# Performance work log

Measured on AMD Instinct MI355X. Metric: run time of the kernel, lower is better.

## Reference

```python
import jax, jax.numpy as jnp
import numpy as np

D_MODEL = 1024
N_HEADS = 16
D_HEAD = D_MODEL // N_HEADS
ROPE_BASE = 10000.0


def setup_inputs() -> dict:
    key = jax.random.key(0)
    k1, k2, k3, k4, k5 = jax.random.split(key, 5)
    std = 0.02 / np.sqrt(2 * 12)  # scaled_xavier with n_layers=12
    x = jax.random.normal(k1, (2, 2048, D_MODEL), dtype=jnp.float32)
    qkv_w = jax.random.normal(k2, (3 * D_MODEL, D_MODEL), dtype=jnp.float32) * std
    qkv_b = jnp.zeros((3 * D_MODEL,), dtype=jnp.float32)
    proj_w = jax.random.normal(k3, (D_MODEL, D_MODEL), dtype=jnp.float32) * std
    proj_b = jnp.zeros((D_MODEL,), dtype=jnp.float32)
    return {"x": x, "qkv_w": qkv_w, "qkv_b": qkv_b, "proj_w": proj_w, "proj_b": proj_b}


def _rope_cos_sin(seq_len, dtype):
    inv_freq = 1.0 / (ROPE_BASE ** (jnp.arange(0, D_HEAD, 2, dtype=jnp.float32) / D_HEAD))
    t = jnp.arange(seq_len, dtype=jnp.float32)
    freqs = jnp.einsum("t,d->td", t, inv_freq)          # [S, Dh/2]
    freqs = jnp.concatenate([freqs, freqs], axis=-1)      # [S, Dh]
    return jnp.cos(freqs).astype(dtype), jnp.sin(freqs).astype(dtype)


def _rotate_half(x):
    x1, x2 = jnp.split(x, 2, axis=-1)
    return jnp.concatenate([-x2, x1], axis=-1)


def reference(x, qkv_w, qkv_b, proj_w, proj_b):
    B, S, D = x.shape
    H, Dh = N_HEADS, D_HEAD
    scale = 1.0 / np.sqrt(Dh)

    qkv = x @ qkv_w.T + qkv_b                              # [B, S, 3D]
    qkv = qkv.reshape(B, S, 3, H, Dh)
    q = jnp.transpose(qkv[:, :, 0], (0, 2, 1, 3))          # [B, H, S, Dh]
    k = jnp.transpose(qkv[:, :, 1], (0, 2, 1, 3))
    v = jnp.transpose(qkv[:, :, 2], (0, 2, 1, 3))

    cos, sin = _rope_cos_sin(S, x.dtype)                   # [S, Dh]
    q = q * cos + _rotate_half(q) * sin
    k = k * cos + _rotate_half(k) * sin

    scores = jnp.einsum("bhsd,bhtd->bhst", q, k) * scale   # [B, H, S, S]
    causal = jnp.triu(jnp.ones((S, S), dtype=bool), k=1)
    neg = jnp.finfo(scores.dtype).min
    scores = jnp.where(causal[None, None], neg, scores)

    probs = jax.nn.softmax(scores, axis=-1)
    ctx = jnp.einsum("bhst,bhtd->bhsd", probs, v)          # [B, H, S, Dh]
    out = jnp.transpose(ctx, (0, 2, 1, 3)).reshape(B, S, D)
    out = out @ proj_w.T + proj_b
    return out
```

## Files before the change

### kernel.cpp

```cpp
#include <hip/hip_runtime.h>
#include <hip/hip_bf16.h>

#define BATCH 2
#define SEQ   2048
#define DMODEL 1024
#define NHEADS 16
#define DHEAD  64
#define MTOT   (BATCH * SEQ)
#define QKSTR  2048

typedef __attribute__((ext_vector_type(8))) short bf16x8;
typedef __attribute__((ext_vector_type(4))) float f32x4;

__device__ __forceinline__ void glds16(const void* g, void* l)
{
    __builtin_amdgcn_global_load_lds(
        (const __attribute__((address_space(1))) unsigned int*)g,
        (__attribute__((address_space(3))) unsigned int*)l, 16, 0, 0);
}

__global__ void cast_all_kernel(
    const float* __restrict__ a, __hip_bfloat16* __restrict__ oa, int na4,
    const float* __restrict__ b, __hip_bfloat16* __restrict__ ob, int nb4,
    const float* __restrict__ c, __hip_bfloat16* __restrict__ oc, int nc4)
{
    int i = blockIdx.x * blockDim.x + threadIdx.x;
    const float* src; __hip_bfloat16* dst; int j = i;
    if (j < na4) { src = a; dst = oa; }
    else {
        j -= na4;
        if (j < nb4) { src = b; dst = ob; }
        else {
            j -= nb4;
            if (j >= nc4) return;
            src = c; dst = oc;
        }
    }
    float4 v = ((const float4*)src)[j];
    __hip_bfloat16 tmp[4];
    tmp[0] = __float2bfloat16(v.x);
    tmp[1] = __float2bfloat16(v.y);
    tmp[2] = __float2bfloat16(v.z);
    tmp[3] = __float2bfloat16(v.w);
    *(uint2*)(dst + 4 * (size_t)j) = *(const uint2*)tmp;
}

#define GTM 128
#define GBK 64

__device__ __forceinline__ void store_out(float* p, float v) { *p = v; }
__device__ __forceinline__ void store_out(__hip_bfloat16* p, float v) { *p = __float2bfloat16(v); }

template <typename OutT, int MODE, int TN>
__global__ __launch_bounds__(256) void gemm_bias_kernel(
    const __hip_bfloat16* __restrict__ A, const __hip_bfloat16* __restrict__ W,
    const float* __restrict__ bias, OutT* __restrict__ out,
    __hip_bfloat16* __restrict__ vtg,
    int M, int N, int K)
{
    const int NI = TN / 32;
    const int bm = blockIdx.x * GTM;
    const int bn = blockIdx.y * TN;
    const int tid = threadIdx.x;
    const int wave = tid >> 6;
    const int lane = tid & 63;
    const int quad = lane >> 4;
    const int l16 = lane & 15;
    const int wm = (wave & 1) * 64;
    const int wn = (wave >> 1) * (TN / 2);

    __shared__ __hip_bfloat16 As[GTM * GBK];
    __shared__ __hip_bfloat16 Bs[TN * GBK];

    f32x4 acc[4][NI] = {};

    const int srow = lane >> 3;
    const int gc8 = (((lane & 7) ^ srow)) * 8;

    for (int kt = 0; kt < K; kt += GBK) {
#pragma unroll
        for (int t = 0; t < 4; t++) {
            int i = wave * 4 + t;
            glds16(A + (size_t)(bm + i * 8 + srow) * K + kt + gc8, As + i * 512);
        }
#pragma unroll
        for (int t = 0; t < TN / 32; t++) {
            int i = wave * (TN / 32) + t;
            glds16(W + (size_t)(bn + i * 8 + srow) * K + kt + gc8, Bs + i * 512);
        }
        __syncthreads();

#pragma unroll
        for (int kk = 0; kk < 2; kk++) {
            bf16x8 af[4], bfr[NI];
#pragma unroll
            for (int i = 0; i < 4; i++) {
                int ra = wm + i * 16 + l16;
                af[i] = *(const bf16x8*)(As + ra * 64 + (((kk << 2) + quad) ^ (ra & 7)) * 8);
            }
#pragma unroll
            for (int i = 0; i < NI; i++) {
                int rb = wn + i * 16 + l16;
                bfr[i] = *(const bf16x8*)(Bs + rb * 64 + (((kk << 2) + quad) ^ (rb & 7)) * 8);
            }
#pragma unroll
            for (int mi = 0; mi < 4; mi++)
#pragma unroll
                for (int ni = 0; ni < NI; ni++)
                    acc[mi][ni] = __builtin_amdgcn_mfma_f32_16x16x32_bf16(
                        af[mi], bfr[ni], acc[mi][ni], 0, 0, 0);
        }
        __syncthreads();
    }

    if (MODE == 1 && (bn + wn) < 2 * DMODEL) {
#pragma unroll
        for (int ni = 0; ni < 2; ni++) {
            int col = bn + wn + ni * 16 + l16;
            int i32 = col & 31;
            float invf = exp2f(-13.287712379549449f * (float)i32 * (1.0f / 32.0f));
            float b1 = bias[col], b2 = bias[col + 32];
#pragma unroll
            for (int mi = 0; mi < 4; mi++) {
#pragma unroll
                for (int r = 0; r < 4; r++) {
                    int row = bm + wm + mi * 16 + quad * 4 + r;
                    int s = row & (SEQ - 1);
                    float ang = (float)s * invf;
                    float sn, cs;
                    __sincosf(ang, &sn, &cs);
                    float x1 = acc[mi][ni][r] + b1;
                    float x2 = acc[mi][ni + 2][r] + b2;
                    store_out(&out[(size_t)row * QKSTR + col], x1 * cs - x2 * sn);
                    store_out(&out[(size_t)row * QKSTR + col + 32], x2 * cs + x1 * sn);
                }
            }
        }
    } else if (MODE == 1) {
#pragma unroll
        for (int ni = 0; ni < NI; ni++) {
            int colg = bn + wn + ni * 16 + l16;
            int vcol = colg - 2 * DMODEL;
            int hh = vcol >> 6, dh = vcol & 63;
            float bv = bias[colg];
#pragma unroll
            for (int mi = 0; mi < 4; mi++) {
                int row0 = bm + wm + mi * 16 + quad * 4;
                int bb = row0 >> 11;
                int ss = row0 & (SEQ - 1);
                __hip_bfloat16 tmp[4];
#pragma unroll
                for (int r = 0; r < 4; r++)
                    tmp[r] = __float2bfloat16(acc[mi][ni][r] + bv);
                *(uint2*)(vtg + (((size_t)bb * NHEADS + hh) * DHEAD + dh) * SEQ + ss) =
                    *(uint2*)tmp;
            }
        }
    } else {
#pragma unroll
        for (int mi = 0; mi < 4; mi++)
#pragma unroll
            for (int ni = 0; ni < NI; ni++) {
                int col = bn + wn + ni * 16 + l16;
                float bv = bias[col];
#pragma unroll
                for (int r = 0; r < 4; r++) {
                    int row = bm + wm + mi * 16 + quad * 4 + r;
                    store_out(&out[(size_t)row * N + col], acc[mi][ni][r] + bv);
                }
            }
    }
}

__global__ __launch_bounds__(512, 2) void flash_attn_mfma_kernel(
    const __hip_bfloat16* __restrict__ qkb,
    const __hip_bfloat16* __restrict__ vtg,
    __hip_bfloat16* __restrict__ ctx)
{
    const int bh = blockIdx.x;
    const int b = bh >> 4, h = bh & 15;
    const int y = blockIdx.y;
    const int qa = y, qb = 15 - y;
    const int tid = threadIdx.x;
    const int w = tid >> 6;
    const int lane = tid & 63;
    const int quad = lane >> 4;
    const int l16 = lane & 15;
    const int band = w & 3;
    const int qt = (w >> 2) ? qb : qa;
    const int jmax_w = 2 * qt + (band >> 1);
    const int jmax_b = 2 * qb + 1;

    __shared__ __hip_bfloat16 Ks[2][64 * 64];
    __shared__ __hip_bfloat16 Vt[2][64 * 64];
    __shared__ __hip_bfloat16 Ps[256 * 64];

    const __hip_bfloat16* qbase = qkb + (size_t)b * SEQ * QKSTR + h * DHEAD;
    const __hip_bfloat16* kbase = qbase + DMODEL;
    const __hip_bfloat16* vbase = vtg + (size_t)bh * DHEAD * SEQ;

    bf16x8 qf[2][2];
#pragma unroll
    for (int mi = 0; mi < 2; mi++) {
        const __hip_bfloat16* qr =
            qbase + (size_t)(qt * 128 + band * 32 + mi * 16 + l16) * QKSTR;
        qf[mi][0] = *(const bf16x8*)(qr + quad * 8);
        qf[mi][1] = *(const bf16x8*)(qr + 32 + quad * 8);
    }

    const int srow = lane >> 3;
    const int gc8 = ((lane & 7) ^ srow) * 8;
    const __hip_bfloat16* kg = kbase + (size_t)(w * 8 + srow) * QKSTR + gc8;
    const __hip_bfloat16* vg = vbase + (size_t)(w * 8 + srow) * SEQ + gc8;

    const int xr = l16 & 7;
    const int fo0 = l16 * 64 + ((quad ^ xr) << 3);
    const int fo1 = l16 * 64 + (((4 + quad) ^ xr) << 3);
    const int pbase = w * 32;

    const short onev = (l16 == 0) ? (short)0x3F80 : (short)0;
    const bf16x8 ones = {onev, onev, onev, onev, onev, onev, onev, onev};

    glds16(kg, &Ks[0][w * 512]);
    glds16(vg, &Vt[0][w * 512]);

    f32x4 oacc[2][5] = {};

    for (int jt = 0; jt <= jmax_b; jt++) {
        __syncthreads();
        const int cur = jt & 1;
        if (jt < jmax_b) {
            glds16(kg + (size_t)(jt + 1) * 64 * QKSTR, &Ks[cur ^ 1][w * 512]);
            glds16(vg + (jt + 1) * 64, &Vt[cur ^ 1][w * 512]);
        }
        if (jt <= jmax_w) {
            const __hip_bfloat16* ks = Ks[cur];
            const __hip_bfloat16* vs = Vt[cur];

            f32x4 s4[2][4] = {};
#pragma unroll
            for (int kk = 0; kk < 2; kk++) {
                const int fo = kk ? fo1 : fo0;
                bf16x8 kf[4];
#pragma unroll
                for (int nt = 0; nt < 4; nt++)
                    kf[nt] = *(const bf16x8*)(ks + nt * 1024 + fo);
#pragma unroll
                for (int mi = 0; mi < 2; mi++)
#pragma unroll
                    for (int nt = 0; nt < 4; nt++)
                        s4[mi][nt] = __builtin_amdgcn_mfma_f32_16x16x32_bf16(
                            qf[mi][kk], kf[nt], s4[mi][nt], 0, 0, 0);
            }

            const int k0 = jt * 64;
#pragma unroll
            for (int mi = 0; mi < 2; mi++) {
                const int qmin = qt * 128 + band * 32 + mi * 16;
                const bool needmask = (k0 + 63) > qmin;
#pragma unroll
                for (int nt = 0; nt < 4; nt++)
#pragma unroll
                    for (int r = 0; r < 4; r++) {
                        float p = __expf(s4[mi][nt][r] * 0.125f);
                        if (needmask)
                            p = (k0 + nt * 16 + l16 <= qmin + quad * 4 + r) ? p : 0.f;
                        int rr = quad * 4 + r;
                        Ps[(pbase + mi * 16 + rr) * 64 +
                           (((nt * 2 + (l16 >> 3)) ^ (rr & 7)) << 3) + xr] =
                            __float2bfloat16(p);
                    }
            }

#pragma unroll
            for (int kk = 0; kk < 2; kk++) {
                const int fo = kk ? fo1 : fo0;
                bf16x8 pf[2];
#pragma unroll
                for (int mi = 0; mi < 2; mi++)
                    pf[mi] = *(const bf16x8*)(Ps + (pbase + mi * 16 + l16) * 64 +
                                              ((((kk << 2) + quad) ^ xr) << 3));
#pragma unroll
                for (int dt = 0; dt < 4; dt++) {
                    bf16x8 vf = *(const bf16x8*)(vs + dt * 1024 + fo);
#pragma unroll
                    for (int mi = 0; mi < 2; mi++)
                        oacc[mi][dt] = __builtin_amdgcn_mfma_f32_16x16x32_bf16(
                            pf[mi], vf, oacc[mi][dt], 0, 0, 0);
                }
#pragma unroll
                for (int mi = 0; mi < 2; mi++)
                    oacc[mi][4] = __builtin_amdgcn_mfma_f32_16x16x32_bf16(
                        pf[mi], ones, oacc[mi][4], 0, 0, 0);
            }
        }
    }

#pragma unroll
    for (int mi = 0; mi < 2; mi++)
#pragma unroll
        for (int r = 0; r < 4; r++) {
            float lv = __shfl(oacc[mi][4][r], lane & 48);
            float il = 1.0f / lv;
            int qg = qt * 128 + band * 32 + mi * 16 + quad * 4 + r;
            __hip_bfloat16* op =
                ctx + (((size_t)b * SEQ + qg) * NHEADS + h) * DHEAD + l16;
#pragma unroll
            for (int dt = 0; dt < 4; dt++)
                op[dt * 16] = __float2bfloat16(oacc[mi][dt][r] * il);
        }
}

extern "C" void kernel_launch(void* const* d_in, const int* in_sizes, int n_in,
                              void* d_out, int out_size, void* d_ws, size_t ws_size,
                              hipStream_t stream)
{
    const float* x      = (const float*)d_in[0];
    const float* qkv_w  = (const float*)d_in[1];
    const float* qkv_b  = (const float*)d_in[2];
    const float* proj_w = (const float*)d_in[3];
    const float* proj_b = (const float*)d_in[4];
    float* out = (float*)d_out;

    char* w = (char*)d_ws;
    __hip_bfloat16* qkb = (__hip_bfloat16*)w;  w += (size_t)MTOT * QKSTR * 2;
    __hip_bfloat16* vtg = (__hip_bfloat16*)w;  w += (size_t)MTOT * DMODEL * 2;
    __hip_bfloat16* ctx = (__hip_bfloat16*)w;  w += (size_t)MTOT * DMODEL * 2;
    __hip_bfloat16* xb  = (__hip_bfloat16*)w;  w += (size_t)MTOT * DMODEL * 2;
    __hip_bfloat16* wqk = (__hip_bfloat16*)w;  w += (size_t)3 * DMODEL * DMODEL * 2;
    __hip_bfloat16* wpr = (__hip_bfloat16*)w;

    const int na4 = MTOT * DMODEL / 4;
    const int nb4 = 3 * DMODEL * DMODEL / 4;
    const int nc4 = DMODEL * DMODEL / 4;

    cast_all_kernel<<<(na4 + nb4 + nc4 + 255) / 256, 256, 0, stream>>>(
        x, xb, na4, qkv_w, wqk, nb4, proj_w, wpr, nc4);

    gemm_bias_kernel<__hip_bfloat16, 1, 128>
        <<<dim3(MTOT / GTM, (3 * DMODEL) / 128), 256, 0, stream>>>(
        xb, wqk, qkv_b, qkb, vtg, MTOT, 3 * DMODEL, DMODEL);

    flash_attn_mfma_kernel<<<dim3(BATCH * NHEADS, 8), 512, 0, stream>>>(qkb, vtg, ctx);

    gemm_bias_kernel<float, 0, 64>
        <<<dim3(MTOT / GTM, DMODEL / 64), 256, 0, stream>>>(
        ctx, wpr, proj_b, out, nullptr, MTOT, DMODEL, DMODEL);
}
```

Baseline: 202.5 us.

## Shrink GEMM M-tile and split attention blocks to one query tile each

```diff
diff --git a/kernel.cpp b/kernel.cpp
--- a/kernel.cpp
+++ b/kernel.cpp
@@ -45,14 +45,14 @@
     *(uint2*)(dst + 4 * (size_t)j) = *(const uint2*)tmp;
 }
 
-#define GTM 128
+#define GTM 64
 #define GBK 64
 
 __device__ __forceinline__ void store_out(float* p, float v) { *p = v; }
 __device__ __forceinline__ void store_out(__hip_bfloat16* p, float v) { *p = __float2bfloat16(v); }
 
 template <typename OutT, int MODE, int TN>
-__global__ __launch_bounds__(256) void gemm_bias_kernel(
+__global__ __launch_bounds__(256, 6) void gemm_bias_kernel(
     const __hip_bfloat16* __restrict__ A, const __hip_bfloat16* __restrict__ W,
     const float* __restrict__ bias, OutT* __restrict__ out,
     __hip_bfloat16* __restrict__ vtg,
@@ -66,21 +66,21 @@
     const int lane = tid & 63;
     const int quad = lane >> 4;
     const int l16 = lane & 15;
-    const int wm = (wave & 1) * 64;
+    const int wm = (wave & 1) * 32;
     const int wn = (wave >> 1) * (TN / 2);
 
     __shared__ __hip_bfloat16 As[GTM * GBK];
     __shared__ __hip_bfloat16 Bs[TN * GBK];
 
-    f32x4 acc[4][NI] = {};
+    f32x4 acc[2][NI] = {};
 
     const int srow = lane >> 3;
     const int gc8 = (((lane & 7) ^ srow)) * 8;
 
     for (int kt = 0; kt < K; kt += GBK) {
 #pragma unroll
-        for (int t = 0; t < 4; t++) {
-            int i = wave * 4 + t;
+        for (int t = 0; t < 2; t++) {
+            int i = wave * 2 + t;
             glds16(A + (size_t)(bm + i * 8 + srow) * K + kt + gc8, As + i * 512);
         }
 #pragma unroll
@@ -92,9 +92,9 @@
 
 #pragma unroll
         for (int kk = 0; kk < 2; kk++) {
-            bf16x8 af[4], bfr[NI];
-#pragma unroll
-            for (int i = 0; i < 4; i++) {
+            bf16x8 af[2], bfr[NI];
+#pragma unroll
+            for (int i = 0; i < 2; i++) {
                 int ra = wm + i * 16 + l16;
                 af[i] = *(const bf16x8*)(As + ra * 64 + (((kk << 2) + quad) ^ (ra & 7)) * 8);
             }
@@ -104,7 +104,7 @@
                 bfr[i] = *(const bf16x8*)(Bs + rb * 64 + (((kk << 2) + quad) ^ (rb & 7)) * 8);
             }
 #pragma unroll
-            for (int mi = 0; mi < 4; mi++)
+            for (int mi = 0; mi < 2; mi++)
 #pragma unroll
                 for (int ni = 0; ni < NI; ni++)
                     acc[mi][ni] = __builtin_amdgcn_mfma_f32_16x16x32_bf16(
@@ -121,7 +121,7 @@
             float invf = exp2f(-13.287712379549449f * (float)i32 * (1.0f / 32.0f));
             float b1 = bias[col], b2 = bias[col + 32];
 #pragma unroll
-            for (int mi = 0; mi < 4; mi++) {
+            for (int mi = 0; mi < 2; mi++) {
 #pragma unroll
                 for (int r = 0; r < 4; r++) {
                     int row = bm + wm + mi * 16 + quad * 4 + r;
@@ -144,7 +144,7 @@
             int hh = vcol >> 6, dh = vcol & 63;
             float bv = bias[colg];
 #pragma unroll
-            for (int mi = 0; mi < 4; mi++) {
+            for (int mi = 0; mi < 2; mi++) {
                 int row0 = bm + wm + mi * 16 + quad * 4;
                 int bb = row0 >> 11;
                 int ss = row0 & (SEQ - 1);
@@ -158,7 +158,7 @@
         }
     } else {
 #pragma unroll
-        for (int mi = 0; mi < 4; mi++)
+        for (int mi = 0; mi < 2; mi++)
 #pragma unroll
             for (int ni = 0; ni < NI; ni++) {
                 int col = bn + wn + ni * 16 + l16;
@@ -172,28 +172,25 @@
     }
 }
 
-__global__ __launch_bounds__(512, 2) void flash_attn_mfma_kernel(
+__global__ __launch_bounds__(256, 3) void flash_attn_mfma_kernel(
     const __hip_bfloat16* __restrict__ qkb,
     const __hip_bfloat16* __restrict__ vtg,
     __hip_bfloat16* __restrict__ ctx)
 {
     const int bh = blockIdx.x;
     const int b = bh >> 4, h = bh & 15;
-    const int y = blockIdx.y;
-    const int qa = y, qb = 15 - y;
+    const int qt = blockIdx.y;
     const int tid = threadIdx.x;
     const int w = tid >> 6;
     const int lane = tid & 63;
     const int quad = lane >> 4;
     const int l16 = lane & 15;
-    const int band = w & 3;
-    const int qt = (w >> 2) ? qb : qa;
-    const int jmax_w = 2 * qt + (band >> 1);
-    const int jmax_b = 2 * qb + 1;
+    const int jmax_w = 2 * qt + (w >> 1);
+    const int jmax_b = 2 * qt + 1;
 
     __shared__ __hip_bfloat16 Ks[2][64 * 64];
     __shared__ __hip_bfloat16 Vt[2][64 * 64];
-    __shared__ __hip_bfloat16 Ps[256 * 64];
+    __shared__ __hip_bfloat16 Ps[128 * 64];
 
     const __hip_bfloat16* qbase = qkb + (size_t)b * SEQ * QKSTR + h * DHEAD;
     const __hip_bfloat16* kbase = qbase + DMODEL;
@@ -203,15 +200,15 @@
 #pragma unroll
     for (int mi = 0; mi < 2; mi++) {
         const __hip_bfloat16* qr =
-            qbase + (size_t)(qt * 128 + band * 32 + mi * 16 + l16) * QKSTR;
+            qbase + (size_t)(qt * 128 + w * 32 + mi * 16 + l16) * QKSTR;
         qf[mi][0] = *(const bf16x8*)(qr + quad * 8);
         qf[mi][1] = *(const bf16x8*)(qr + 32 + quad * 8);
     }
 
     const int srow = lane >> 3;
     const int gc8 = ((lane & 7) ^ srow) * 8;
-    const __hip_bfloat16* kg = kbase + (size_t)(w * 8 + srow) * QKSTR + gc8;
-    const __hip_bfloat16* vg = vbase + (size_t)(w * 8 + srow) * SEQ + gc8;
+    const __hip_bfloat16* kg = kbase + (size_t)(w * 16 + srow) * QKSTR + gc8;
+    const __hip_bfloat16* vg = vbase + (size_t)(w * 16 + srow) * SEQ + gc8;
 
     const int xr = l16 & 7;
     const int fo0 = l16 * 64 + ((quad ^ xr) << 3);
@@ -221,8 +218,10 @@
     const short onev = (l16 == 0) ? (short)0x3F80 : (short)0;
     const bf16x8 ones = {onev, onev, onev, onev, onev, onev, onev, onev};
 
-    glds16(kg, &Ks[0][w * 512]);
-    glds16(vg, &Vt[0][w * 512]);
+    glds16(kg, &Ks[0][w * 1024]);
+    glds16(kg + 8 * QKSTR, &Ks[0][w * 1024 + 512]);
+    glds16(vg, &Vt[0][w * 1024]);
+    glds16(vg + 8 * SEQ, &Vt[0][w * 1024 + 512]);
 
     f32x4 oacc[2][5] = {};
 
@@ -230,8 +229,14 @@
         __syncthreads();
         const int cur = jt & 1;
         if (jt < jmax_b) {
-            glds16(kg + (size_t)(jt + 1) * 64 * QKSTR, &Ks[cur ^ 1][w * 512]);
-            glds16(vg + (jt + 1) * 64, &Vt[cur ^ 1][w * 512]);
+            const __hip_bfloat16* kn = kg + (size_t)(jt + 1) * 64 * QKSTR;
+            const __hip_bfloat16* vn = vg + (jt + 1) * 64;
+            __hip_bfloat16* kd = &Ks[cur ^ 1][w * 1024];
+            __hip_bfloat16* vd = &Vt[cur ^ 1][w * 1024];
+            glds16(kn, kd);
+            glds16(kn + 8 * QKSTR, kd + 512);
+            glds16(vn, vd);
+            glds16(vn + 8 * SEQ, vd + 512);
         }
         if (jt <= jmax_w) {
             const __hip_bfloat16* ks = Ks[cur];
@@ -256,7 +261,7 @@
             const int k0 = jt * 64;
 #pragma unroll
             for (int mi = 0; mi < 2; mi++) {
-                const int qmin = qt * 128 + band * 32 + mi * 16;
+                const int qmin = qt * 128 + w * 32 + mi * 16;
                 const bool needmask = (k0 + 63) > qmin;
 #pragma unroll
                 for (int nt = 0; nt < 4; nt++)
@@ -302,7 +307,7 @@
         for (int r = 0; r < 4; r++) {
             float lv = __shfl(oacc[mi][4][r], lane & 48);
             float il = 1.0f / lv;
-            int qg = qt * 128 + band * 32 + mi * 16 + quad * 4 + r;
+            int qg = qt * 128 + w * 32 + mi * 16 + quad * 4 + r;
             __hip_bfloat16* op =
                 ctx + (((size_t)b * SEQ + qg) * NHEADS + h) * DHEAD + l16;
 #pragma unroll
@@ -341,7 +346,8 @@
         <<<dim3(MTOT / GTM, (3 * DMODEL) / 128), 256, 0, stream>>>(
         xb, wqk, qkv_b, qkb, vtg, MTOT, 3 * DMODEL, DMODEL);
 
-    flash_attn_mfma_kernel<<<dim3(BATCH * NHEADS, 8), 512, 0, stream>>>(qkb, vtg, ctx);
+    flash_attn_mfma_kernel<<<dim3(BATCH * NHEADS, SEQ / 128), 256, 0, stream>>>(
+        qkb, vtg, ctx);
 
     gemm_bias_kernel<float, 0, 64>
         <<<dim3(MTOT / GTM, DMODEL / 64), 256, 0, stream>>>(
```

After: 191.9 us. 5.2% less time.
